# Kernel optimization log

Hardware: AMD Instinct MI355X
Metric: run time of the kernel (lower is better)

The kernel has to match this reference:

```python
import jax, jax.numpy as jnp
import numpy as np

CHAR_EMB = 30
CHAR_HID = 100  # bidirectional -> 50 per direction
HID = CHAR_HID // 2
VOCAB = 100
B, S, T = 64, 256, 16


def setup_inputs() -> dict:
    key = jax.random.key(0)
    ks = jax.random.split(key, 10)
    char_ids = jax.random.randint(ks[0], (B, S, T), 0, VOCAB, dtype=jnp.int64)
    scale = np.sqrt(3.0 / CHAR_EMB)
    emb = jax.random.uniform(ks[1], (VOCAB, CHAR_EMB), minval=-scale, maxval=scale, dtype=jnp.float32)
    # torch LSTM param layout: w_ih [4H, in], w_hh [4H, H], gate order i,f,g,o
    k = 1.0 / np.sqrt(HID)
    def u(kk, shape):
        return jax.random.uniform(kk, shape, minval=-k, maxval=k, dtype=jnp.float32)
    return {
        "char_ids": char_ids,
        "emb": emb,
        "w_ih_f": u(ks[2], (4 * HID, CHAR_EMB)), "w_hh_f": u(ks[3], (4 * HID, HID)),
        "b_ih_f": u(ks[4], (4 * HID,)), "b_hh_f": u(ks[5], (4 * HID,)),
        "w_ih_r": u(ks[6], (4 * HID, CHAR_EMB)), "w_hh_r": u(ks[7], (4 * HID, HID)),
        "b_ih_r": u(ks[8], (4 * HID,)), "b_hh_r": u(ks[9], (4 * HID,)),
    }


def _lstm_scan(x, w_ih, w_hh, b_ih, b_hh):
    # x: [N, T, E] -> outputs ys [T, N, H], final h [N, H]
    N = x.shape[0]
    xw = jnp.einsum('nte,ge->ntg', x, w_ih) + (b_ih + b_hh)  # [N, T, 4H]
    xw = jnp.transpose(xw, (1, 0, 2))  # [T, N, 4H]

    def step(carry, xt):
        h, c = carry
        gates = xt + h @ w_hh.T
        i, f, g, o = jnp.split(gates, 4, axis=-1)
        i = jax.nn.sigmoid(i); f = jax.nn.sigmoid(f)
        g = jnp.tanh(g); o = jax.nn.sigmoid(o)
        c = f * c + i * g
        h = o * jnp.tanh(c)
        return (h, c), h

    h0 = jnp.zeros((N, HID), x.dtype)
    (hT, _), ys = jax.lax.scan(step, (h0, h0), xw)
    return ys, hT


def reference(char_ids, emb, w_ih_f, w_hh_f, b_ih_f, b_hh_f,
              w_ih_r, w_hh_r, b_ih_r, b_hh_r):
    b, s, t = char_ids.shape
    ids = char_ids.reshape(b * s, t)                 # [N, T]
    lengths = (ids != 0).sum(axis=1)                 # ragged lengths (pad id 0)
    x = emb[ids]                                     # [N, T, E]; dropout = identity (eval)

    # forward direction: need hidden at position lengths-1
    ys_f, _ = _lstm_scan(x, w_ih_f, w_hh_f, b_ih_f, b_hh_f)   # [T, N, H]
    ys_f = jnp.transpose(ys_f, (1, 0, 2))                      # [N, T, H]
    idx = jnp.maximum(lengths - 1, 0)[:, None, None]           # guard all-pad rows
    h_fwd = jnp.take_along_axis(ys_f, idx, axis=1)[:, 0, :]    # [N, H]

    # backward direction: output at t=0 == final carry of reversed scan
    _, h_bwd = _lstm_scan(x[:, ::-1, :], w_ih_r, w_hh_r, b_ih_r, b_hh_r)  # [N, H]

    out = jnp.concatenate([h_fwd, h_bwd], axis=-1)   # [N, 2H]
    return out.reshape(b, s, CHAR_HID)
```

## Files before the change

kernel.cpp:

```cpp
#include <hip/hip_runtime.h>

#define T 16
#define E 30
#define H 50
#define VOCAB 100
#define NSEQ 16384
#define ROWS 208

typedef _Float16 v8hf __attribute__((ext_vector_type(8)));
typedef float v4f __attribute__((ext_vector_type(4)));

__global__ void build_tbl(const float* __restrict__ emb,
                          const float* __restrict__ w_ih,
                          const float* __restrict__ b_ih,
                          const float* __restrict__ b_hh,
                          float* __restrict__ tbl) {
    int idx = blockIdx.x * blockDim.x + threadIdx.x;
    if (idx >= VOCAB * ROWS) return;
    int v = idx / ROWS, r = idx % ROWS;
    float s = 0.f;
    if (r < 4 * H) {
        int orig = (r & 3) * H + (r >> 2);
        s = b_ih[orig] + b_hh[orig];
        const float* er = emb + v * E;
        const float* wr = w_ih + orig * E;
#pragma unroll
        for (int e = 0; e < E; ++e) s += er[e] * wr[e];
    }
    tbl[idx] = s;
}

__device__ __forceinline__ float rcpf(float x) { return __builtin_amdgcn_rcpf(x); }
__device__ __forceinline__ float sigm(float x) { return rcpf(1.0f + __expf(-x)); }
__device__ __forceinline__ float ftanh(float x) {
    float e = __expf(2.0f * x);
    return (e - 1.0f) * rcpf(e + 1.0f);
}

#define HL_STRIDE  (16 * 56)
#define BUF_STRIDE (2 * 2 * 16 * 56)
#define GRP_STRIDE (2 * 16 * 56)

template<int RT0, int NT>
__device__ __forceinline__ void run_half(
    const float* __restrict__ whh, const float* __restrict__ tb,
    const int* __restrict__ myids, _Float16* __restrict__ hb0,
    float* __restrict__ out, int seq, int dir, int capt, int l15, int lg)
{
    v8hf afrag[NT][2];
#pragma unroll
    for (int i = 0; i < NT; ++i) {
        const int r = (RT0 + i) * 16 + l15;
        const bool vr = (r < 4 * H);
        const int orig = vr ? ((r & 3) * H + (r >> 2)) : 0;
#pragma unroll
        for (int kh = 0; kh < 2; ++kh) {
            v8hf af;
#pragma unroll
            for (int j = 0; j < 8; ++j) {
                const int k = kh * 32 + lg * 8 + j;
                af[j] = (_Float16)((vr && k < H) ? whh[orig * H + k] : 0.f);
            }
            afrag[i][kh] = af;
        }
    }
    float cst[NT];
#pragma unroll
    for (int i = 0; i < NT; ++i) cst[i] = 0.f;

    const int roff = l15 * 56 + lg * 8;
    const int woff = l15 * 56 + RT0 * 4 + lg;

    int id_next = myids[dir ? (T - 1) : 0];

    for (int t = 0; t < T; ++t) {
        const int cur = t & 1, nxt = cur ^ 1;
        const int id = id_next;
        if (t < T - 1) id_next = myids[dir ? (T - 2 - t) : (t + 1)];
        const float* __restrict__ trow = tb + id * ROWS;

        const _Float16* rb = hb0 + cur * BUF_STRIDE;
        v8hf bh0 = *(const v8hf*)(rb + roff);
        v8hf bh1 = *(const v8hf*)(rb + roff + 32);
        v8hf bl0 = *(const v8hf*)(rb + HL_STRIDE + roff);
        v8hf bl1 = *(const v8hf*)(rb + HL_STRIDE + roff + 32);

        _Float16* wb = hb0 + nxt * BUF_STRIDE + woff;

#pragma unroll
        for (int i = 0; i < NT; ++i) {
            const int rt = RT0 + i;
            v4f c = *(const v4f*)(trow + rt * 16 + lg * 4);
            c = __builtin_amdgcn_mfma_f32_16x16x32_f16(afrag[i][0], bh0, c, 0, 0, 0);
            c = __builtin_amdgcn_mfma_f32_16x16x32_f16(afrag[i][1], bh1, c, 0, 0, 0);
            c = __builtin_amdgcn_mfma_f32_16x16x32_f16(afrag[i][0], bl0, c, 0, 0, 0);
            c = __builtin_amdgcn_mfma_f32_16x16x32_f16(afrag[i][1], bl1, c, 0, 0, 0);

            float i_ = sigm(c[0]);
            float f_ = sigm(c[1]);
            float g_ = ftanh(c[2]);
            float o_ = sigm(c[3]);
            float cn = fmaf(f_, cst[i], i_ * g_);
            cst[i] = cn;
            float hn = o_ * ftanh(cn);

            const int u = rt * 4 + lg;
            if (u < H) {
                _Float16 hi = (_Float16)hn;
                wb[i * 4] = hi;
                wb[HL_STRIDE + i * 4] = (_Float16)(hn - (float)hi);
                if (t == capt) out[seq * 100 + dir * H + u] = hn;
            }
        }
        __syncthreads();
    }
}

__global__ __launch_bounds__(256, 4) void lstm_mfma(
    const int* __restrict__ ids,
    const float* __restrict__ tbl,
    const float* __restrict__ whh_f,
    const float* __restrict__ whh_r,
    float* __restrict__ out)
{
    __shared__ _Float16 hbuf[2][2][2][16][56];

    const int tid = threadIdx.x;
    const int lane = tid & 63;
    const int wave = tid >> 6;
    const int grp = wave >> 1;
    const int half = wave & 1;
    const int l15 = lane & 15;
    const int lg = lane >> 4;
    const int b = blockIdx.x;
    const int dir = b >> 9;
    const int seq = (b & 511) * 32 + grp * 16 + l15;

    const float* __restrict__ whh = dir ? whh_r : whh_f;
    const float* __restrict__ tb  = tbl + dir * (VOCAB * ROWS);
    const int* __restrict__ myids = ids + seq * T;

    {
        int* hz = (int*)&hbuf[0][0][0][0][0];
#pragma unroll
        for (int i = tid; i < (int)(sizeof(hbuf) / 4); i += 256) hz[i] = 0;
    }

    int capt;
    {
        const int4* q = (const int4*)myids;
        int4 a0 = q[0], a1 = q[1], a2 = q[2], a3 = q[3];
        int len = (a0.x != 0) + (a0.y != 0) + (a0.z != 0) + (a0.w != 0)
                + (a1.x != 0) + (a1.y != 0) + (a1.z != 0) + (a1.w != 0)
                + (a2.x != 0) + (a2.y != 0) + (a2.z != 0) + (a2.w != 0)
                + (a3.x != 0) + (a3.y != 0) + (a3.z != 0) + (a3.w != 0);
        capt = dir ? (T - 1) : ((len > 1) ? (len - 1) : 0);
    }

    __syncthreads();

    _Float16* hb0 = &hbuf[0][grp][0][0][0];
    if (half == 0)
        run_half<0, 7>(whh, tb, myids, hb0, out, seq, dir, capt, l15, lg);
    else
        run_half<7, 6>(whh, tb, myids, hb0, out, seq, dir, capt, l15, lg);
}

extern "C" void kernel_launch(void* const* d_in, const int* in_sizes, int n_in,
                              void* d_out, int out_size, void* d_ws, size_t ws_size,
                              hipStream_t stream) {
    const int*   char_ids = (const int*)d_in[0];
    const float* emb      = (const float*)d_in[1];
    const float* w_ih_f   = (const float*)d_in[2];
    const float* w_hh_f   = (const float*)d_in[3];
    const float* b_ih_f   = (const float*)d_in[4];
    const float* b_hh_f   = (const float*)d_in[5];
    const float* w_ih_r   = (const float*)d_in[6];
    const float* w_hh_r   = (const float*)d_in[7];
    const float* b_ih_r   = (const float*)d_in[8];
    const float* b_hh_r   = (const float*)d_in[9];
    float* out = (float*)d_out;
    float* tbl = (float*)d_ws;

    const int nt = VOCAB * ROWS;
    build_tbl<<<(nt + 255) / 256, 256, 0, stream>>>(emb, w_ih_f, b_ih_f, b_hh_f, tbl);
    build_tbl<<<(nt + 255) / 256, 256, 0, stream>>>(emb, w_ih_r, b_ih_r, b_hh_r, tbl + nt);
    lstm_mfma<<<1024, 256, 0, stream>>>(char_ids, tbl, w_hh_f, w_hh_r, out);
}
```

Before: 77.20 us.

## Split LSTM gate rows across four waves and prescale gates for exp2

Each block now handles one 16-sequence group, with its 13 gate-row tiles spread over four waves instead of two. The grid doubles to 2048 blocks and launch bounds rise to 6 blocks per CU, which shortens each wave's serial per-timestep chain and adds parallelism. The table and recurrent weights are pre-scaled by -log2(e) or 2*log2(e), so the activations can use native exp2 with no extra multiply. The captured hidden state is kept in registers and written once after the loop rather than conditionally inside it. In exchange, each wave reloads its full h fragments every step for fewer tiles, and more waves share each barrier.

```diff
diff --git a/kernel.cpp b/kernel.cpp
--- a/kernel.cpp
+++ b/kernel.cpp
@@ -4,11 +4,16 @@
 #define E 30
 #define H 50
 #define VOCAB 100
-#define NSEQ 16384
 #define ROWS 208
+#define K1 1.44269504089f
+#define K2 2.88539008178f
 
 typedef _Float16 v8hf __attribute__((ext_vector_type(8)));
 typedef float v4f __attribute__((ext_vector_type(4)));
+
+extern "C" __device__ float __ocml_native_exp2_f32(float);
+__device__ __forceinline__ float e2(float x)   { return __ocml_native_exp2_f32(x); }
+__device__ __forceinline__ float rcpf(float x) { return __builtin_amdgcn_rcpf(x); }
 
 __global__ void build_tbl(const float* __restrict__ emb,
                           const float* __restrict__ w_ih,
@@ -26,23 +31,16 @@
         const float* wr = w_ih + orig * E;
 #pragma unroll
         for (int e = 0; e < E; ++e) s += er[e] * wr[e];
+        s *= ((r & 3) == 2) ? K2 : -K1;
     }
     tbl[idx] = s;
 }
 
-__device__ __forceinline__ float rcpf(float x) { return __builtin_amdgcn_rcpf(x); }
-__device__ __forceinline__ float sigm(float x) { return rcpf(1.0f + __expf(-x)); }
-__device__ __forceinline__ float ftanh(float x) {
-    float e = __expf(2.0f * x);
-    return (e - 1.0f) * rcpf(e + 1.0f);
-}
-
 #define HL_STRIDE  (16 * 56)
-#define BUF_STRIDE (2 * 2 * 16 * 56)
-#define GRP_STRIDE (2 * 16 * 56)
+#define BUF_STRIDE (2 * 16 * 56)
 
 template<int RT0, int NT>
-__device__ __forceinline__ void run_half(
+__device__ __forceinline__ void run_part(
     const float* __restrict__ whh, const float* __restrict__ tb,
     const int* __restrict__ myids, _Float16* __restrict__ hb0,
     float* __restrict__ out, int seq, int dir, int capt, int l15, int lg)
@@ -53,20 +51,21 @@
         const int r = (RT0 + i) * 16 + l15;
         const bool vr = (r < 4 * H);
         const int orig = vr ? ((r & 3) * H + (r >> 2)) : 0;
+        const float sc = ((r & 3) == 2) ? K2 : -K1;
 #pragma unroll
         for (int kh = 0; kh < 2; ++kh) {
             v8hf af;
 #pragma unroll
             for (int j = 0; j < 8; ++j) {
                 const int k = kh * 32 + lg * 8 + j;
-                af[j] = (_Float16)((vr && k < H) ? whh[orig * H + k] : 0.f);
+                af[j] = (_Float16)((vr && k < H) ? sc * whh[orig * H + k] : 0.f);
             }
             afrag[i][kh] = af;
         }
     }
-    float cst[NT];
+    float cs[NT], hcap[NT];
 #pragma unroll
-    for (int i = 0; i < NT; ++i) cst[i] = 0.f;
+    for (int i = 0; i < NT; ++i) { cs[i] = 0.f; hcap[i] = 0.f; }
 
     const int roff = l15 * 56 + lg * 8;
     const int woff = l15 * 56 + RT0 * 4 + lg;
@@ -86,6 +85,7 @@
         v8hf bl1 = *(const v8hf*)(rb + HL_STRIDE + roff + 32);
 
         _Float16* wb = hb0 + nxt * BUF_STRIDE + woff;
+        const bool cap = (t == capt);
 
 #pragma unroll
         for (int i = 0; i < NT; ++i) {
@@ -96,52 +96,57 @@
             c = __builtin_amdgcn_mfma_f32_16x16x32_f16(afrag[i][0], bl0, c, 0, 0, 0);
             c = __builtin_amdgcn_mfma_f32_16x16x32_f16(afrag[i][1], bl1, c, 0, 0, 0);
 
-            float i_ = sigm(c[0]);
-            float f_ = sigm(c[1]);
-            float g_ = ftanh(c[2]);
-            float o_ = sigm(c[3]);
-            float cn = fmaf(f_, cst[i], i_ * g_);
-            cst[i] = cn;
-            float hn = o_ * ftanh(cn);
+            float i_ = rcpf(1.f + e2(c[0]));
+            float f_ = rcpf(1.f + e2(c[1]));
+            float eg = e2(c[2]);
+            float g_ = (eg - 1.f) * rcpf(eg + 1.f);
+            float o_ = rcpf(1.f + e2(c[3]));
+            cs[i] = fmaf(f_, cs[i], (i_ * g_) * K2);
+            float ec = e2(cs[i]);
+            float th = (ec - 1.f) * rcpf(ec + 1.f);
+            float hn = o_ * th;
 
-            const int u = rt * 4 + lg;
-            if (u < H) {
+            if (rt != 12 || lg < 2) {
                 _Float16 hi = (_Float16)hn;
                 wb[i * 4] = hi;
                 wb[HL_STRIDE + i * 4] = (_Float16)(hn - (float)hi);
-                if (t == capt) out[seq * 100 + dir * H + u] = hn;
+                hcap[i] = cap ? hn : hcap[i];
             }
         }
         __syncthreads();
     }
+
+#pragma unroll
+    for (int i = 0; i < NT; ++i) {
+        const int u = (RT0 + i) * 4 + lg;
+        if (u < H) out[seq * 100 + dir * H + u] = hcap[i];
+    }
 }
 
-__global__ __launch_bounds__(256, 4) void lstm_mfma(
+__global__ __launch_bounds__(256, 6) void lstm_mfma(
     const int* __restrict__ ids,
     const float* __restrict__ tbl,
     const float* __restrict__ whh_f,
     const float* __restrict__ whh_r,
     float* __restrict__ out)
 {
-    __shared__ _Float16 hbuf[2][2][2][16][56];
+    __shared__ _Float16 hbuf[2][2][16][56];
 
     const int tid = threadIdx.x;
     const int lane = tid & 63;
     const int wave = tid >> 6;
-    const int grp = wave >> 1;
-    const int half = wave & 1;
     const int l15 = lane & 15;
     const int lg = lane >> 4;
     const int b = blockIdx.x;
-    const int dir = b >> 9;
-    const int seq = (b & 511) * 32 + grp * 16 + l15;
+    const int dir = b >> 10;
+    const int seq = (b & 1023) * 16 + l15;
 
     const float* __restrict__ whh = dir ? whh_r : whh_f;
     const float* __restrict__ tb  = tbl + dir * (VOCAB * ROWS);
     const int* __restrict__ myids = ids + seq * T;
 
     {
-        int* hz = (int*)&hbuf[0][0][0][0][0];
+        int* hz = (int*)&hbuf[0][0][0][0];
 #pragma unroll
         for (int i = tid; i < (int)(sizeof(hbuf) / 4); i += 256) hz[i] = 0;
     }
@@ -159,11 +164,11 @@
 
     __syncthreads();
 
-    _Float16* hb0 = &hbuf[0][grp][0][0][0];
-    if (half == 0)
-        run_half<0, 7>(whh, tb, myids, hb0, out, seq, dir, capt, l15, lg);
-    else
-        run_half<7, 6>(whh, tb, myids, hb0, out, seq, dir, capt, l15, lg);
+    _Float16* hb0 = &hbuf[0][0][0][0];
+    if      (wave == 0) run_part<0, 3>(whh, tb, myids, hb0, out, seq, dir, capt, l15, lg);
+    else if (wave == 1) run_part<3, 3>(whh, tb, myids, hb0, out, seq, dir, capt, l15, lg);
+    else if (wave == 2) run_part<6, 3>(whh, tb, myids, hb0, out, seq, dir, capt, l15, lg);
+    else                run_part<9, 4>(whh, tb, myids, hb0, out, seq, dir, capt, l15, lg);
 }
 
 extern "C" void kernel_launch(void* const* d_in, const int* in_sizes, int n_in,
@@ -185,5 +190,5 @@
     const int nt = VOCAB * ROWS;
     build_tbl<<<(nt + 255) / 256, 256, 0, stream>>>(emb, w_ih_f, b_ih_f, b_hh_f, tbl);
     build_tbl<<<(nt + 255) / 256, 256, 0, stream>>>(emb, w_ih_r, b_ih_r, b_hh_r, tbl + nt);
-    lstm_mfma<<<1024, 256, 0, stream>>>(char_ids, tbl, w_hh_f, w_hh_r, out);
+    lstm_mfma<<<2048, 256, 0, stream>>>(char_ids, tbl, w_hh_f, w_hh_r, out);
 }
```

New measurement: 113.4 us. 46.8% more time.
